# Performance work log

Hardware: AMD Instinct MI355X
Metric: run time of the kernel (lower is better)

Reference implementation:

```python
import jax, jax.numpy as jnp
import numpy as np

B, D, C, F = 1024, 8192, 345, 512
PROTO_W = 0.99  # args.proto_m


def setup_inputs() -> dict:
    key = jax.random.key(0)
    k = jax.random.split(key, 6)
    img_q = jax.random.normal(k[0], (B, D), jnp.float32)
    img_q1 = jax.random.normal(k[1], (B, D), jnp.float32)
    # partial label mask: random candidate set, guarantee >=1 candidate per row
    partial_Y = (jax.random.uniform(k[2], (B, C)) < 0.3).astype(jnp.float32)
    partial_Y = partial_Y.at[jnp.arange(B), jnp.arange(B) % C].set(1.0)
    W_enc = jax.random.normal(k[3], (D, F), jnp.float32) / np.sqrt(D).astype(np.float32)
    W_fc = jax.random.normal(k[4], (F, C), jnp.float32) / np.sqrt(F).astype(np.float32)
    b_fc = jnp.zeros((C,), jnp.float32)
    proto = jax.random.normal(k[5], (C, F), jnp.float32)
    proto = proto / jnp.linalg.norm(proto, axis=1, keepdims=True)
    return {"img_q": img_q, "img_q1": img_q1, "partial_Y": partial_Y,
            "W_enc": W_enc, "W_fc": W_fc, "b_fc": b_fc, "proto": proto}


def reference(img_q, img_q1, partial_Y, W_enc, W_fc, b_fc, proto):
    # encoder: feats [B,F], logits [B,C] (abstracted backbone + shared fc)
    feats_q = img_q @ W_enc
    logits_q = feats_q @ W_fc + b_fc
    feats_q1 = img_q1 @ W_enc
    logits_q1 = feats_q1 @ W_fc + b_fc

    # partial-label restricted pseudo labels
    scores = jax.nn.softmax(logits_q, axis=1) * partial_Y
    scores = scores / scores.sum(axis=1, keepdims=True)
    labels = jnp.argmax(scores, axis=1)  # [B] int

    # Sequential per-sample EMA p[l] = w*p[l] + (1-w)*f, vectorized in closed form.
    # For a sample with c_after same-label samples occurring later, its final
    # contribution is (1-w)*w^c_after * f; the old prototype is scaled by w^count.
    onehot = jax.nn.one_hot(labels, C, dtype=feats_q.dtype)   # [B,C]
    cum = jnp.cumsum(onehot, axis=0)                          # inclusive counts
    occ = cum[jnp.arange(B), labels] - 1.0                    # occurrences before i
    total = cum[-1]                                           # [C] per-class counts
    c_after = total[labels] - occ - 1.0                       # [B]
    coef = (1.0 - PROTO_W) * PROTO_W ** c_after               # [B]
    contrib = jax.ops.segment_sum(coef[:, None] * feats_q, labels, num_segments=C)
    new_proto = (PROTO_W ** total)[:, None] * proto + contrib
    new_proto = new_proto / jnp.linalg.norm(new_proto, axis=1, keepdims=True)

    prot_scores = new_proto @ W_fc + b_fc
    return logits_q, logits_q1, new_proto, prot_scores, labels, feats_q, feats_q1
```

## Files before the change

### kernel.cpp

```cpp
#include <hip/hip_runtime.h>
#include <float.h>
#include <math.h>

#define B_SZ 1024
#define D_SZ 8192
#define C_SZ 345
#define F_SZ 512
#define PROTO_W 0.99f


#define WS_XH 0
#define WS_XL 33554432u
#define WS_WH 67108864u
#define WS_WL 75497472u
#define WS_P  83886080u
#define WS2_WFH 100663296u
#define WS2_WFL 101056512u
#define WS2_LAB 101449728u
#define WS2_NEED 101457920u
#define WS2_FH 0u
#define WS2_FL 2097152u

#define WS_NEED 92274688u
#define WS_FH  0u
#define WS_FL  2097152u
// ... 41 lines not shown
    do {                                                                 \
        bf16x8 a0h = *(const bf16x8*)&sAh[IA0];                          \
        bf16x8 a1h = *(const bf16x8*)&sAh[IA1];                          \
        bf16x8 b0h = *(const bf16x8*)&sBh[IB0];                          \
        bf16x8 b1h = *(const bf16x8*)&sBh[IB1];                          \
        bf16x8 a0l = *(const bf16x8*)&sAl[IA0];                          \
        bf16x8 a1l = *(const bf16x8*)&sAl[IA1];                          \
        bf16x8 b0l = *(const bf16x8*)&sBl[IB0];                          \
        bf16x8 b1l = *(const bf16x8*)&sBl[IB1];                          \
        acc[0][0] = MFMA_BF16(a0h, b0h, acc[0][0], 0, 0, 0);             \
        acc[0][1] = MFMA_BF16(a0h, b1h, acc[0][1], 0, 0, 0);             \
        acc[1][0] = MFMA_BF16(a1h, b0h, acc[1][0], 0, 0, 0);             \
        acc[1][1] = MFMA_BF16(a1h, b1h, acc[1][1], 0, 0, 0);             \
        acc[0][0] = MFMA_BF16(a0h, b0l, acc[0][0], 0, 0, 0);             \
        acc[0][1] = MFMA_BF16(a0h, b1l, acc[0][1], 0, 0, 0);             \
        acc[1][0] = MFMA_BF16(a1h, b0l, acc[1][0], 0, 0, 0);             \
        acc[1][1] = MFMA_BF16(a1h, b1l, acc[1][1], 0, 0, 0);             \
        acc[0][0] = MFMA_BF16(a0l, b0h, acc[0][0], 0, 0, 0);             \
        acc[0][1] = MFMA_BF16(a0l, b1h, acc[0][1], 0, 0, 0);             \
        acc[1][0] = MFMA_BF16(a1l, b0h, acc[1][0], 0, 0, 0);             \
        acc[1][1] = MFMA_BF16(a1l, b1h, acc[1][1], 0, 0, 0);             \
    } while (0)

__global__ __launch_bounds__(256) void convert_all(
    const float* __restrict__ img_q, const float* __restrict__ img_q1,
    const float* __restrict__ W_enc, const float* __restrict__ W_fc,
    short* __restrict__ Xh, short* __restrict__ Xl,
    short* __restrict__ Wh, short* __restrict__ Wl,
    short* __restrict__ Wth, short* __restrict__ Wtl)
{
    __shared__ float tile[64][65];
    const int bid = blockIdx.x;
    const int t = threadIdx.x;

    if (bid < 1024) {
        const int HALF = (B_SZ * D_SZ) / 4;
        const int total = 2 * HALF;
        for (int i4 = bid * 256 + t; i4 < total; i4 += 1024 * 256) {
            float4 v = (i4 < HALF) ? ((const float4*)img_q)[i4]
                                   : ((const float4*)img_q1)[i4 - HALF];
            short4v h, l;
            short hh, ll;
            split_bf16(v.x, hh, ll); h.x = hh; l.x = ll;
            split_bf16(v.y, hh, ll); h.y = hh; l.y = ll;
            split_bf16(v.z, hh, ll); h.z = hh; l.z = ll;
            split_bf16(v.w, hh, ll); h.w = hh; l.w = ll;
            ((short4v*)Xh)[i4] = h;
            ((short4v*)Xl)[i4] = l;
        }
    } else if (bid < 2048) {
        const int id = bid - 1024;
        const int k0 = (id >> 3) * 64;
        const int n0 = (id & 7) * 64;
        {
            const int kr = t >> 2;
            const int cb = (t & 3) * 16;
// ... 30 lines not shown
            const int kr = idx >> 6;
            const int cc = idx & 63;
            tile[kr][cc] = (c0 + cc < C_SZ) ? W_fc[(size_t)(k0 + kr) * C_SZ + c0 + cc] : 0.0f;
        }
        __syncthreads();
        const int crow = t >> 2;
#pragma unroll
        for (int cc2 = 0; cc2 < 2; ++cc2) {
            const int ch = (t & 3) * 2 + cc2;
            short8v h, l;
#pragma unroll
            for (int e = 0; e < 8; ++e) {
                short hh, ll;
                split_bf16(tile[ch * 8 + e][crow], hh, ll);
                h[e] = hh; l[e] = ll;
            }
            size_t off = (size_t)(c0 + crow) * F_SZ + k0 + ch * 8;
            *(short8v*)&Wth[off] = h;
            *(short8v*)&Wtl[off] = l;
        }
    }
}

__global__ __launch_bounds__(512, 1) void gemm_ws128_v3(
    const short* __restrict__ Xh, const short* __restrict__ Xl,
    const short* __restrict__ Wh, const short* __restrict__ Wl,
    float* __restrict__ P, int ksteps)
{
    __shared__ __align__(16) short sAh[2][8192];
    __shared__ __align__(16) short sAl[2][8192];
    __shared__ __align__(16) short sBh[2][8192];
    __shared__ __align__(16) short sBl[2][8192];

    const int t = threadIdx.x;
    const int lane = t & 63;
    const int wave = t >> 6;

    const int flat = blockIdx.x + 4 * blockIdx.y + 64 * blockIdx.z;
    const int logical = (flat & 7) * 32 + (flat >> 3);
    const int nt = logical & 3;
    const int mt = (logical >> 2) & 15;
    const int ks = logical >> 6;

    const int m0 = mt * 128;
    const int n0 = nt * 128;
    const int kbase = ks * ksteps * 64;

    const int arr = wave >> 1;
    const int half = wave & 1;
    const short* gbase =
        (arr == 0) ? Xh + (size_t)m0 * D_SZ :
        (arr == 1) ? Xl + (size_t)m0 * D_SZ :
        (arr == 2) ? Wh + (size_t)n0 * D_SZ :
                     Wl + (size_t)n0 * D_SZ;
    short* lb[2];
    lb[0] = ((arr == 0) ? sAh[0] : (arr == 1) ? sAl[0] : (arr == 2) ? sBh[0] : sBl[0]) + half * 4096;
    lb[1] = ((arr == 0) ? sAh[1] : (arr == 1) ? sAl[1] : (arr == 2) ? sBh[1] : sBl[1]) + half * 4096;
    const int lrow8 = lane >> 3;
    const int gchunkOff = ((lane & 7) ^ lrow8) * 8;
    const short* gsrc = gbase + (size_t)(half * 64 + lrow8) * D_SZ + kbase + gchunkOff;

    const int wr = wave >> 2;
    const int wc = wave & 3;
    const int mo = wr * 64;
    const int no = wc * 32;
    const int lr = lane & 15;
    const int lkg = lane >> 4;
    const int x7 = lr & 7;
    const int sl0 = lkg ^ x7;
    const int sl1 = (4 + lkg) ^ x7;
    int aoff[4], boff[2];
#pragma unroll
    for (int f = 0; f < 4; ++f) aoff[f] = (mo + 16 * f + lr) * 64;
#pragma unroll
    for (int g = 0; g < 2; ++g) boff[g] = (no + 16 * g + lr) * 64;

    f32x4 acc[4][2] = {};

#pragma unroll
    for (int j = 0; j < 8; ++j)
        gl_lds16(gsrc + (size_t)(8 * j) * D_SZ, lb[0] + j * 512);

    int buf = 0;
    for (int s = 0; s < ksteps; ++s) {
        if (s + 1 < ksteps) {
            short* dst = lb[buf ^ 1];
            const short* g = gsrc + (s + 1) * 64;
#pragma unroll
            for (int j = 0; j < 8; ++j)
                gl_lds16(g + (size_t)(8 * j) * D_SZ, dst + j * 512);
            asm volatile("s_waitcnt vmcnt(8)" ::: "memory");
        } else {
            asm volatile("s_waitcnt vmcnt(0)" ::: "memory");
        }
        fence_barrier();

        const short* pAh = sAh[buf];
        const short* pAl = sAl[buf];
        const short* pBh = sBh[buf];
        const short* pBl = sBl[buf];

        {
            bf16x8 ah[4], al[4], bh[2], bl_[2];
#pragma unroll
            for (int f = 0; f < 4; ++f) {
                ah[f] = *(const bf16x8*)&pAh[aoff[f] + sl0 * 8];
                al[f] = *(const bf16x8*)&pAl[aoff[f] + sl0 * 8];
            }
#pragma unroll
            for (int g = 0; g < 2; ++g) {
                bh[g]  = *(const bf16x8*)&pBh[boff[g] + sl0 * 8];
                bl_[g] = *(const bf16x8*)&pBl[boff[g] + sl0 * 8];
            }
            __builtin_amdgcn_s_setprio(1);
#pragma unroll
            for (int f = 0; f < 4; ++f)
#pragma unroll
                for (int g = 0; g < 2; ++g)
                    acc[f][g] = MFMA_BF16(ah[f], bh[g], acc[f][g], 0, 0, 0);
#pragma unroll
            for (int f = 0; f < 4; ++f)
#pragma unroll
                for (int g = 0; g < 2; ++g)
                    acc[f][g] = MFMA_BF16(ah[f], bl_[g], acc[f][g], 0, 0, 0);
#pragma unroll
            for (int f = 0; f < 4; ++f)
#pragma unroll
                for (int g = 0; g < 2; ++g)
                    acc[f][g] = MFMA_BF16(al[f], bh[g], acc[f][g], 0, 0, 0);
            __builtin_amdgcn_s_setprio(0);
        }
        fence_barrier();

        {
            bf16x8 ah[4], al[4], bh[2], bl_[2];
#pragma unroll
            for (int f = 0; f < 4; ++f) {
                ah[f] = *(const bf16x8*)&pAh[aoff[f] + sl1 * 8];
                al[f] = *(const bf16x8*)&pAl[aoff[f] + sl1 * 8];
            }
#pragma unroll
            for (int g = 0; g < 2; ++g) {
                bh[g]  = *(const bf16x8*)&pBh[boff[g] + sl1 * 8];
                bl_[g] = *(const bf16x8*)&pBl[boff[g] + sl1 * 8];
            }
            __builtin_amdgcn_s_setprio(1);
#pragma unroll
            for (int f = 0; f < 4; ++f)
#pragma unroll
                for (int g = 0; g < 2; ++g)
                    acc[f][g] = MFMA_BF16(ah[f], bh[g], acc[f][g], 0, 0, 0);
#pragma unroll
            for (int f = 0; f < 4; ++f)
#pragma unroll
                for (int g = 0; g < 2; ++g)
                    acc[f][g] = MFMA_BF16(ah[f], bl_[g], acc[f][g], 0, 0, 0);
#pragma unroll
            for (int f = 0; f < 4; ++f)
#pragma unroll
                for (int g = 0; g < 2; ++g)
                    acc[f][g] = MFMA_BF16(al[f], bh[g], acc[f][g], 0, 0, 0);
            __builtin_amdgcn_s_setprio(0);
        }
        fence_barrier();
        buf ^= 1;
    }

    float* Pout = P + (size_t)ks * (2048u * 512u);
#pragma unroll
    for (int f = 0; f < 4; ++f)
#pragma unroll
        for (int g = 0; g < 2; ++g) {
            const int col  = n0 + no + 16 * g + (lane & 15);
            const int row0 = m0 + mo + 16 * f + (lane >> 4) * 4;
#pragma unroll
            for (int r = 0; r < 4; ++r)
                Pout[(size_t)(row0 + r) * F_SZ + col] = acc[f][g][r];
        }
}

__global__ __launch_bounds__(256, 1) void gemm_ws128(
    const short* __restrict__ Xh, const short* __restrict__ Xl,
    const short* __restrict__ Wh, const short* __restrict__ Wl,
    float* __restrict__ P, int ksteps)
{
    __shared__ __align__(16) short sAh[2][8192];
    __shared__ __align__(16) short sAl[2][8192];
    __shared__ __align__(16) short sBh[2][8192];
    __shared__ __align__(16) short sBl[2][8192];

    const int t = threadIdx.x;
    const int lane = t & 63;
    const int wave = t >> 6;
    const int nt = blockIdx.x;
    const int mt = blockIdx.y;
    const int ks = blockIdx.z;
    const int m0 = mt * 128;
    const int n0 = nt * 128;
    const int kbase = ks * ksteps * 64;

    const short* gbase =
        (wave == 0) ? Xh + (size_t)m0 * D_SZ :
        (wave == 1) ? Xl + (size_t)m0 * D_SZ :
// ... 73 lines not shown
#pragma unroll
                for (int f = 0; f < 4; ++f)
#pragma unroll
                    for (int g = 0; g < 4; ++g)
                        acc[f][g] = MFMA_BF16(al[f], bh[g], acc[f][g], 0, 0, 0);
            }
        }
        __builtin_amdgcn_s_setprio(0);
        fence_barrier();
        buf ^= 1;
    }

    float* Pout = P + (size_t)ks * (2048u * 512u);
#pragma unroll
    for (int f = 0; f < 4; ++f)
#pragma unroll
        for (int g = 0; g < 4; ++g) {
            const int col  = n0 + no + 16 * g + (lane & 15);
            const int row0 = m0 + mo + 16 * f + (lane >> 4) * 4;
#pragma unroll
            for (int r = 0; r < 4; ++r)
                Pout[(size_t)(row0 + r) * F_SZ + col] = acc[f][g][r];
        }
}

__global__ __launch_bounds__(256) void reduce_feats4(
    const float* __restrict__ P, float* __restrict__ feats,
    short* __restrict__ Fh, short* __restrict__ Fl)
{
    const int i4 = blockIdx.x * 256 + threadIdx.x;
    float4 a = ((const float4*)P)[i4];
#pragma unroll
    for (int sl = 1; sl < 4; ++sl) {
        float4 b = ((const float4*)(P + (size_t)sl * (2048u * 512u)))[i4];
        a.x += b.x; a.y += b.y; a.z += b.z; a.w += b.w;
    }
    ((float4*)feats)[i4] = a;
    float v[4] = {a.x, a.y, a.z, a.w};
    short4v h, l;
    short hh, ll;
#pragma unroll
    for (int e = 0; e < 4; ++e) {
        split_bf16(v[e], hh, ll); h[e] = hh; l[e] = ll;
    }
    ((short4v*)Fh)[i4] = h;
    ((short4v*)Fl)[i4] = l;
}

__global__ __launch_bounds__(256, 2) void fc_logits3(
    const short* __restrict__ Ah, const short* __restrict__ Al,
    const short* __restrict__ Bh_g, const short* __restrict__ Bl_g,
    const float* __restrict__ bias, const float* __restrict__ partial_Y,
    float* __restrict__ logits, unsigned long long* __restrict__ labPack)
{
    __shared__ __align__(16) short dAh[2][4096];
    __shared__ __align__(16) short dAl[2][4096];
    __shared__ __align__(16) short dBh[2][4096];
    __shared__ __align__(16) short dBl[2][4096];

    const int t = threadIdx.x;
    const int lane = t & 63;
    const int wave = t >> 6;
    const int n0 = blockIdx.x * 64;
    const int m0 = blockIdx.y * 64;

    const int lrow8 = lane >> 3;
    const int colOff = ((lane & 7) ^ lrow8) * 8;

    const short* gsrc = (wave == 0) ? Ah : (wave == 1) ? Al
                      : (wave == 2) ? Bh_g : Bl_g;
    const int rbase = (wave < 2) ? m0 : n0;
    short* lb[2];
    lb[0] = (wave == 0) ? dAh[0] : (wave == 1) ? dAl[0] : (wave == 2) ? dBh[0] : dBl[0];
    lb[1] = (wave == 0) ? dAh[1] : (wave == 1) ? dAl[1] : (wave == 2) ? dBh[1] : dBl[1];
    const short* gbase = gsrc + (size_t)(rbase + lrow8) * F_SZ + colOff;

    const int mo = (wave >> 1) * 32;
    const int no = (wave & 1) * 32;
    const int lr = lane & 15;
    const int lkg = lane >> 4;
    const int x7 = lr & 7;
    const int sl0 = (0 + lkg) ^ x7;
    const int sl1 = (4 + lkg) ^ x7;
    const int ra0 = (mo + lr) * 64,      ra1 = (mo + 16 + lr) * 64;
    const int rb0 = (no + lr) * 64,      rb1 = (no + 16 + lr) * 64;
    const int a00 = ra0 + sl0 * 8, a01 = ra0 + sl1 * 8;
    const int a10 = ra1 + sl0 * 8, a11 = ra1 + sl1 * 8;
    const int b00 = rb0 + sl0 * 8, b01 = rb0 + sl1 * 8;
    const int b10 = rb1 + sl0 * 8, b11 = rb1 + sl1 * 8;

    f32x4 acc[2][2] = {};

#pragma unroll
    for (int j = 0; j < 8; ++j)
        gl_lds16(gbase + (size_t)(8 * j) * F_SZ, lb[0] + j * 512);

    int buf = 0;
    for (int s = 0; s < 8; ++s) {
        if (s + 1 < 8) {
            short* dst = lb[buf ^ 1];
            const short* g = gbase + (s + 1) * 64;
#pragma unroll
            for (int j = 0; j < 8; ++j)
                gl_lds16(g + (size_t)(8 * j) * F_SZ, dst + j * 512);
            asm volatile("s_waitcnt vmcnt(8)" ::: "memory");
        } else {
            asm volatile("s_waitcnt vmcnt(0)" ::: "memory");
        }
        fence_barrier();
        __builtin_amdgcn_s_setprio(1);
        {
            const short* sAh = dAh[buf];
            const short* sAl = dAl[buf];
            const short* sBh = dBh[buf];
            const short* sBl = dBl[buf];
            MFMA_BLOCK(a00, a10, b00, b10);
            MFMA_BLOCK(a01, a11, b01, b11);
        }
        __builtin_amdgcn_s_setprio(0);
        fence_barrier();
        buf ^= 1;
    }

    const bool doArg = (m0 < B_SZ);
#pragma unroll
    for (int f = 0; f < 2; ++f) {
#pragma unroll
        for (int r = 0; r < 4; ++r) {
            const int row = m0 + mo + f * 16 + (lane >> 4) * 4 + r;
            unsigned long long best = 0;
#pragma unroll
            for (int g = 0; g < 2; ++g) {
                const int col = n0 + no + g * 16 + (lane & 15);
                if (col < C_SZ) {
                    const float v = acc[f][g][r] + bias[col];
                    logits[(size_t)row * C_SZ + col] = v;
                    if (doArg && partial_Y[(size_t)row * C_SZ + col] != 0.0f) {
                        unsigned long long p = ((unsigned long long)f2key(v) << 32)
                                             | (unsigned long long)(0xFFFFFFFFu - (unsigned)col);
                        if (p > best) best = p;
                    }
                }
            }
            if (doArg) {
#pragma unroll
                for (int m = 1; m < 16; m <<= 1) {
                    unsigned long long o = __shfl_xor(best, m);
                    if (o > best) best = o;
                }
                if ((lane & 15) == 0 && best != 0)
                    atomicMax(&labPack[row], best);
            }
        }
    }
}

__global__ __launch_bounds__(512) void proto_scores_fused(
    const unsigned long long* __restrict__ labPack,
    const float* __restrict__ feats_q,
    const float* __restrict__ proto,
    const short* __restrict__ Wth, const short* __restrict__ Wtl,
    const float* __restrict__ b_fc,
    float* __restrict__ new_proto, float* __restrict__ scores,
    float* __restrict__ labels_f)
{
    __shared__ int rowlist[B_SZ];
    __shared__ int mcount_s;
    __shared__ float nprow[F_SZ];
    __shared__ float red[8];
    __shared__ float rinv_s;
    const int c = blockIdx.x;
    const int t = threadIdx.x;
    const int lane = t & 63;
    const int w = t >> 6;

    if (c == 0) {
#pragma unroll
        for (int j = 0; j < 2; ++j) {
            const int i = t + j * 512;
            int li = (int)(0xFFFFFFFFu - (unsigned)(labPack[i] & 0xFFFFFFFFull));
            labels_f[i] = (float)li;
        }
    }

    if (w == 0) {
        int k = 0;
#pragma unroll
        for (int ch = 0; ch < 16; ++ch) {
            unsigned long long pk = labPack[ch * 64 + lane];
            int li = (int)(0xFFFFFFFFu - (unsigned)(pk & 0xFFFFFFFFull));
            unsigned long long mask = __ballot(li == c);
            if (lane == 0) {
                while (mask) {
                    int p = __builtin_ctzll(mask);
                    mask &= mask - 1;
                    rowlist[k++] = ch * 64 + p;
                }
            }
            k = __shfl(k, 0);
        }
        if (lane == 0) mcount_s = k;
    }
    __syncthreads();
    const int m = mcount_s;

    float val = proto[(size_t)c * F_SZ + t];
    for (int k = 0; k < m; ++k)
        val = PROTO_W * val + (1.0f - PROTO_W) * feats_q[(size_t)rowlist[k] * F_SZ + t];

    float sq = val * val;
#pragma unroll
    for (int off = 32; off; off >>= 1) sq += __shfl_down(sq, off);
    if ((t & 63) == 0) red[t >> 6] = sq;
    __syncthreads();
    if (t == 0) {
        float s = 0.0f;
#pragma unroll
        for (int ww = 0; ww < 8; ++ww) s += red[ww];
        rinv_s = 1.0f / sqrtf(s);
    }
    __syncthreads();
    const float v = val * rinv_s;
    new_proto[(size_t)c * F_SZ + t] = v;
    nprow[t] = v;
    __syncthreads();

    float np8[8];
#pragma unroll
    for (int j = 0; j < 8; ++j) np8[j] = nprow[lane * 8 + j];
    for (int col = w; col < C_SZ; col += 8) {
        const short8v h = *(const short8v*)&Wth[(size_t)col * F_SZ + lane * 8];
        const short8v l = *(const short8v*)&Wtl[(size_t)col * F_SZ + lane * 8];
        float p = 0.0f;
#pragma unroll
        for (int j = 0; j < 8; ++j)
            p += np8[j] * (bf16_f32(h[j]) + bf16_f32(l[j]));
#pragma unroll
        for (int off = 32; off; off >>= 1) p += __shfl_down(p, off);
        if (lane == 0) scores[(size_t)c * C_SZ + col] = p + b_fc[col];
    }
}

__global__ __launch_bounds__(256) void reduce_feats_split(
    const float* __restrict__ P, float* __restrict__ feats,
    short* __restrict__ Fh, short* __restrict__ Fl,
    const float* __restrict__ W_fc,
    short* __restrict__ Wth, short* __restrict__ Wtl)
{
    const int bid = blockIdx.x;
    const int t = threadIdx.x;
    if (bid < 1024) {
        const int n4 = (2048 * 512) / 4;
        const float* P1 = P + 2048 * 512;
        for (int i4 = bid * 256 + t; i4 < n4; i4 += 1024 * 256) {
            float4 a = ((const float4*)P)[i4];
            float4 b = ((const float4*)P1)[i4];
            float v[4] = {a.x + b.x, a.y + b.y, a.z + b.z, a.w + b.w};
            short4v h, l;
            short hh, ll;
#pragma unroll
            for (int e = 0; e < 4; ++e) {
                feats[i4 * 4 + e] = v[e];
                split_bf16(v[e], hh, ll); h[e] = hh; l[e] = ll;
// ... 183 lines not shown
    const float* proto     = (const float*)d_in[6];

    float* out       = (float*)d_out;
    float* logits    = out;
    float* new_proto = out + 706560;
    float* scores    = out + 883200;
    float* labels_f  = out + 1002225;
    float* feats     = out + 1003249;

    char* ws = (char*)d_ws;
    short* Xh = (short*)(ws + WS_XH);
    short* Xl = (short*)(ws + WS_XL);
    short* Wh = (short*)(ws + WS_WH);
    short* Wl = (short*)(ws + WS_WL);
    float* P  = (float*)(ws + WS_P);

    if (ws_size >= (size_t)WS2_NEED) {
        short* Wth = (short*)(ws + WS2_WFH);
        short* Wtl = (short*)(ws + WS2_WFL);
        unsigned long long* labPack = (unsigned long long*)(ws + WS2_LAB);
        short* Fh = (short*)(ws + WS2_FH);
        short* Fl = (short*)(ws + WS2_FL);

        hipMemsetAsync(labPack, 0, B_SZ * sizeof(unsigned long long), stream);
        hipLaunchKernelGGL(convert_all, dim3(2096), dim3(256), 0, stream,
                           img_q, img_q1, W_enc, W_fc, Xh, Xl, Wh, Wl, Wth, Wtl);
        hipLaunchKernelGGL(gemm_ws128_v3, dim3(4, 16, 4), dim3(512), 0, stream,
                           Xh, Xl, Wh, Wl, P, 32);
        hipLaunchKernelGGL(reduce_feats4, dim3(1024), dim3(256), 0, stream,
                           P, feats, Fh, Fl);
        hipLaunchKernelGGL(fc_logits3, dim3(6, 32), dim3(256), 0, stream,
                           Fh, Fl, Wth, Wtl, b_fc, partial_Y, logits, labPack);
        hipLaunchKernelGGL(proto_scores_fused, dim3(345), dim3(512), 0, stream,
                           labPack, feats, proto, Wth, Wtl, b_fc,
                           new_proto, scores, labels_f);
    } else {
        short* Fh  = (short*)(ws + WS_FH);
        short* Fl  = (short*)(ws + WS_FL);
        short* Wth = (short*)(ws + WS_WFH);
        short* Wtl = (short*)(ws + WS_WFL);
        short* NPh = (short*)(ws + WS_NPH);
        short* NPl = (short*)(ws + WS_NPL);

        hipLaunchKernelGGL(convert_all, dim3(2048), dim3(256), 0, stream,
                           img_q, img_q1, W_enc, W_fc, Xh, Xl, Wh, Wl,
                           (short*)nullptr, (short*)nullptr);
        hipLaunchKernelGGL(gemm_ws128, dim3(4, 16, 2), dim3(256), 0, stream,
                           Xh, Xl, Wh, Wl, P, 64);
        hipLaunchKernelGGL(reduce_feats_split, dim3(1072), dim3(256), 0, stream,
                           P, feats, Fh, Fl, W_fc, Wth, Wtl);
        hipLaunchKernelGGL(gemm_fc, dim3(6, 32), dim3(256), 0, stream,
                           Fh, Fl, Wth, Wtl, b_fc, logits, 2048);
        hipLaunchKernelGGL(argmax_labels, dim3(1024), dim3(64), 0, stream,
                           logits, partial_Y, labels_f);
        hipLaunchKernelGGL(proto_update, dim3(345), dim3(512), 0, stream,
                           labels_f, feats, proto, new_proto, NPh, NPl);
        hipLaunchKernelGGL(gemm_fc, dim3(6, 6), dim3(256), 0, stream,
                           NPh, NPl, Wth, Wtl, b_fc, scores, C_SZ);
    }
}
```

Baseline: 248.2 us.

## Fuse pipeline into single cooperative persistent kernel with grid syncs

Replaces the memset plus five separate launches (convert, split-K GEMM, reduce, fc logits/argmax, proto update/scores) with one cooperative kernel of 256 blocks that separates stages with grid.sync. This removes per-launch overhead and inter-kernel gaps. The cost is that each stage is limited to 256 blocks of 512 threads with one block per CU. The conversion and reduce phases lose the wider grids they had before, and the grid-wide barriers add latency of their own.

```diff
diff --git a/kernel.cpp b/kernel.cpp
--- a/kernel.cpp
+++ b/kernel.cpp
@@ -1,6 +1,9 @@
 #include <hip/hip_runtime.h>
+#include <hip/hip_cooperative_groups.h>
 #include <float.h>
 #include <math.h>
+
+namespace cg = cooperative_groups;
 
 #define B_SZ 1024
 #define D_SZ 8192
@@ -88,16 +91,503 @@
         acc[1][1] = MFMA_BF16(a1l, b1h, acc[1][1], 0, 0, 0);             \
     } while (0)
 
+__device__ __forceinline__ void proto_one(
+    int c, int t, int lane, int w,
+    const unsigned long long* labPack, const float* feats_q,
+    const float* proto_in, const short* Wth, const short* Wtl,
+    const float* b_fc, float* new_proto, float* scores, float* labels_f,
+    int* rowlist, float* nprow, float* red, int* mcount, float* rinv)
+{
+    if (c == 0) {
+#pragma unroll
+        for (int j = 0; j < 2; ++j) {
+            const int i = t + j * 512;
+            int li = (int)(0xFFFFFFFFu - (unsigned)(labPack[i] & 0xFFFFFFFFull));
+            labels_f[i] = (float)li;
+        }
+    }
+
+    if (w == 0) {
+        int k = 0;
+#pragma unroll
+        for (int ch = 0; ch < 16; ++ch) {
+            unsigned long long pk = labPack[ch * 64 + lane];
+            int li = (int)(0xFFFFFFFFu - (unsigned)(pk & 0xFFFFFFFFull));
+            unsigned long long mask = __ballot(li == c);
+            if (lane == 0) {
+                while (mask) {
+                    int p = __builtin_ctzll(mask);
+                    mask &= mask - 1;
+                    rowlist[k++] = ch * 64 + p;
+                }
+            }
+            k = __shfl(k, 0);
+        }
+        if (lane == 0) *mcount = k;
+    }
+    __syncthreads();
+    const int m = *mcount;
+
+    float val = proto_in[(size_t)c * F_SZ + t];
+    for (int k = 0; k < m; ++k)
+        val = PROTO_W * val + (1.0f - PROTO_W) * feats_q[(size_t)rowlist[k] * F_SZ + t];
+
+    float sq = val * val;
+#pragma unroll
+    for (int off = 32; off; off >>= 1) sq += __shfl_down(sq, off);
+    if ((t & 63) == 0) red[t >> 6] = sq;
+    __syncthreads();
+    if (t == 0) {
+        float s = 0.0f;
+#pragma unroll
+        for (int ww = 0; ww < 8; ++ww) s += red[ww];
+        *rinv = 1.0f / sqrtf(s);
+    }
+    __syncthreads();
+    const float v = val * (*rinv);
+    new_proto[(size_t)c * F_SZ + t] = v;
+    nprow[t] = v;
+    __syncthreads();
+
+    float np8[8];
+#pragma unroll
+    for (int j = 0; j < 8; ++j) np8[j] = nprow[lane * 8 + j];
+    for (int col = w; col < C_SZ; col += 8) {
+        const short8v h = *(const short8v*)&Wth[(size_t)col * F_SZ + lane * 8];
+        const short8v l = *(const short8v*)&Wtl[(size_t)col * F_SZ + lane * 8];
+        float p = 0.0f;
+#pragma unroll
+        for (int j = 0; j < 8; ++j)
+            p += np8[j] * (bf16_f32(h[j]) + bf16_f32(l[j]));
+#pragma unroll
+        for (int off = 32; off; off >>= 1) p += __shfl_down(p, off);
+        if (lane == 0) scores[(size_t)c * C_SZ + col] = p + b_fc[col];
+    }
+}
+
+__global__ __launch_bounds__(512, 1) void mega(
+    const float* img_q, const float* img_q1, const float* partial_Y,
+    const float* W_enc, const float* W_fc, const float* b_fc,
+    const float* proto_in,
+    short* Xh, short* Xl, short* Wh, short* Wl, float* P,
+    short* Wth, short* Wtl, unsigned long long* labPack,
+    short* Fh, short* Fl,
+    float* logits, float* new_proto, float* scores, float* labels_f,
+    float* feats)
+{
+    cg::grid_group grid = cg::this_grid();
+    __shared__ __align__(16) char LDSU[131072];
+
+    const int bid = blockIdx.x;
+    const int t = threadIdx.x;
+    const int lane = t & 63;
+    const int wave = t >> 6;
+
+    if (bid < 2) labPack[bid * 512 + t] = 0ull;
+
+    {
+        const int HALF = (B_SZ * D_SZ) / 4;
+        const int total = 2 * HALF;
+        for (int i4 = bid * 512 + t; i4 < total; i4 += 256 * 512) {
+            float4 v = (i4 < HALF) ? ((const float4*)img_q)[i4]
+                                   : ((const float4*)img_q1)[i4 - HALF];
+            short4v h, l;
+            short hh, ll;
+            split_bf16(v.x, hh, ll); h.x = hh; l.x = ll;
+            split_bf16(v.y, hh, ll); h.y = hh; l.y = ll;
+            split_bf16(v.z, hh, ll); h.z = hh; l.z = ll;
+            split_bf16(v.w, hh, ll); h.w = hh; l.w = ll;
+            ((short4v*)Xh)[i4] = h;
+            ((short4v*)Xl)[i4] = l;
+        }
+    }
+
+    {
+        float (*tile)[65] = (float(*)[65])LDSU;
+        const int kr = t >> 3;
+        const int cb = (t & 7) * 8;
+        const int n  = t >> 3;
+        const int ch = t & 7;
+#pragma unroll
+        for (int j = 0; j < 4; ++j) {
+            const int id = bid * 4 + j;
+            const int k0 = (id >> 3) * 64;
+            const int n0 = (id & 7) * 64;
+            __syncthreads();
+            float4 v0 = *(const float4*)&W_enc[(size_t)(k0 + kr) * F_SZ + n0 + cb];
+            float4 v1 = *(const float4*)&W_enc[(size_t)(k0 + kr) * F_SZ + n0 + cb + 4];
+            tile[kr][cb + 0] = v0.x; tile[kr][cb + 1] = v0.y;
+            tile[kr][cb + 2] = v0.z; tile[kr][cb + 3] = v0.w;
+            tile[kr][cb + 4] = v1.x; tile[kr][cb + 5] = v1.y;
+            tile[kr][cb + 6] = v1.z; tile[kr][cb + 7] = v1.w;
+            __syncthreads();
+            short8v h, l;
+#pragma unroll
+            for (int e = 0; e < 8; ++e) {
+                short hh, ll;
+                split_bf16(tile[ch * 8 + e][n], hh, ll);
+                h[e] = hh; l[e] = ll;
+            }
+            size_t off = (size_t)(n0 + n) * D_SZ + k0 + ch * 8;
+            *(short8v*)&Wh[off] = h;
+            *(short8v*)&Wl[off] = l;
+        }
+    }
+
+    if (bid < 48) {
+        float (*tile)[65] = (float(*)[65])LDSU;
+        const int k0 = (bid & 7) * 64;
+        const int c0 = (bid >> 3) * 64;
+        __syncthreads();
+        for (int idx = t; idx < 64 * 64; idx += 512) {
+            const int kr2 = idx >> 6;
+            const int cc = idx & 63;
+            tile[kr2][cc] = (c0 + cc < C_SZ) ? W_fc[(size_t)(k0 + kr2) * C_SZ + c0 + cc] : 0.0f;
+        }
+        __syncthreads();
+        const int crow = t >> 3;
+        const int ch2 = t & 7;
+        short8v h, l;
+#pragma unroll
+        for (int e = 0; e < 8; ++e) {
+            short hh, ll;
+            split_bf16(tile[ch2 * 8 + e][crow], hh, ll);
+            h[e] = hh; l[e] = ll;
+        }
+        size_t off = (size_t)(c0 + crow) * F_SZ + k0 + ch2 * 8;
+        *(short8v*)&Wth[off] = h;
+        *(short8v*)&Wtl[off] = l;
+    }
+
+    asm volatile("s_waitcnt vmcnt(0)" ::: "memory");
+    __threadfence();
+    grid.sync();
+
+    {
+        short (*sAh)[8192] = (short(*)[8192])(LDSU + 0);
+        short (*sAl)[8192] = (short(*)[8192])(LDSU + 32768);
+        short (*sBh)[8192] = (short(*)[8192])(LDSU + 65536);
+        short (*sBl)[8192] = (short(*)[8192])(LDSU + 98304);
+        const int ksteps = 32;
+
+        const int logical = (bid & 7) * 32 + (bid >> 3);
+        const int nt = logical & 3;
+        const int mt = (logical >> 2) & 15;
+        const int ks = logical >> 6;
+
+        const int m0 = mt * 128;
+        const int n0 = nt * 128;
+        const int kbase = ks * ksteps * 64;
+
+        const int arr = wave >> 1;
+        const int half = wave & 1;
+        const short* gbase =
+            (arr == 0) ? Xh + (size_t)m0 * D_SZ :
+            (arr == 1) ? Xl + (size_t)m0 * D_SZ :
+            (arr == 2) ? Wh + (size_t)n0 * D_SZ :
+                         Wl + (size_t)n0 * D_SZ;
+        short* lb[2];
+        lb[0] = ((arr == 0) ? sAh[0] : (arr == 1) ? sAl[0] : (arr == 2) ? sBh[0] : sBl[0]) + half * 4096;
+        lb[1] = ((arr == 0) ? sAh[1] : (arr == 1) ? sAl[1] : (arr == 2) ? sBh[1] : sBl[1]) + half * 4096;
+        const int lrow8 = lane >> 3;
+        const int gchunkOff = ((lane & 7) ^ lrow8) * 8;
+        const short* gsrc = gbase + (size_t)(half * 64 + lrow8) * D_SZ + kbase + gchunkOff;
+
+        const int wr = wave >> 2;
+        const int wc = wave & 3;
+        const int mo = wr * 64;
+        const int no = wc * 32;
+        const int lr = lane & 15;
+        const int lkg = lane >> 4;
+        const int x7 = lr & 7;
+        const int sl0 = lkg ^ x7;
+        const int sl1 = (4 + lkg) ^ x7;
+        int aoff[4], boff[2];
+#pragma unroll
+        for (int f = 0; f < 4; ++f) aoff[f] = (mo + 16 * f + lr) * 64;
+#pragma unroll
+        for (int g = 0; g < 2; ++g) boff[g] = (no + 16 * g + lr) * 64;
+
+        f32x4 acc[4][2] = {};
+
+#pragma unroll
+        for (int j = 0; j < 8; ++j)
+            gl_lds16(gsrc + (size_t)(8 * j) * D_SZ, lb[0] + j * 512);
+
+        int buf = 0;
+        for (int s = 0; s < ksteps; ++s) {
+            if (s + 1 < ksteps) {
+                short* dst = lb[buf ^ 1];
+                const short* g = gsrc + (s + 1) * 64;
+#pragma unroll
+                for (int j = 0; j < 8; ++j)
+                    gl_lds16(g + (size_t)(8 * j) * D_SZ, dst + j * 512);
+                asm volatile("s_waitcnt vmcnt(8)" ::: "memory");
+            } else {
+                asm volatile("s_waitcnt vmcnt(0)" ::: "memory");
+            }
+            fence_barrier();
+
+            const short* pAh = sAh[buf];
+            const short* pAl = sAl[buf];
+            const short* pBh = sBh[buf];
+            const short* pBl = sBl[buf];
+
+            {
+                bf16x8 ah[4], al[4], bh[2], bl_[2];
+#pragma unroll
+                for (int f = 0; f < 4; ++f) {
+                    ah[f] = *(const bf16x8*)&pAh[aoff[f] + sl0 * 8];
+                    al[f] = *(const bf16x8*)&pAl[aoff[f] + sl0 * 8];
+                }
+#pragma unroll
+                for (int g = 0; g < 2; ++g) {
+                    bh[g]  = *(const bf16x8*)&pBh[boff[g] + sl0 * 8];
+                    bl_[g] = *(const bf16x8*)&pBl[boff[g] + sl0 * 8];
+                }
+                __builtin_amdgcn_s_setprio(1);
+#pragma unroll
+                for (int f = 0; f < 4; ++f)
+#pragma unroll
+                    for (int g = 0; g < 2; ++g)
+                        acc[f][g] = MFMA_BF16(ah[f], bh[g], acc[f][g], 0, 0, 0);
+#pragma unroll
+                for (int f = 0; f < 4; ++f)
+#pragma unroll
+                    for (int g = 0; g < 2; ++g)
+                        acc[f][g] = MFMA_BF16(ah[f], bl_[g], acc[f][g], 0, 0, 0);
+#pragma unroll
+                for (int f = 0; f < 4; ++f)
+#pragma unroll
+                    for (int g = 0; g < 2; ++g)
+                        acc[f][g] = MFMA_BF16(al[f], bh[g], acc[f][g], 0, 0, 0);
+                __builtin_amdgcn_s_setprio(0);
+            }
+            fence_barrier();
+
+            {
+                bf16x8 ah[4], al[4], bh[2], bl_[2];
+#pragma unroll
+                for (int f = 0; f < 4; ++f) {
+                    ah[f] = *(const bf16x8*)&pAh[aoff[f] + sl1 * 8];
+                    al[f] = *(const bf16x8*)&pAl[aoff[f] + sl1 * 8];
+                }
+#pragma unroll
+                for (int g = 0; g < 2; ++g) {
+                    bh[g]  = *(const bf16x8*)&pBh[boff[g] + sl1 * 8];
+                    bl_[g] = *(const bf16x8*)&pBl[boff[g] + sl1 * 8];
+                }
+                __builtin_amdgcn_s_setprio(1);
+#pragma unroll
+                for (int f = 0; f < 4; ++f)
+#pragma unroll
+                    for (int g = 0; g < 2; ++g)
+                        acc[f][g] = MFMA_BF16(ah[f], bh[g], acc[f][g], 0, 0, 0);
+#pragma unroll
+                for (int f = 0; f < 4; ++f)
+#pragma unroll
+                    for (int g = 0; g < 2; ++g)
+                        acc[f][g] = MFMA_BF16(ah[f], bl_[g], acc[f][g], 0, 0, 0);
+#pragma unroll
+                for (int f = 0; f < 4; ++f)
+#pragma unroll
+                    for (int g = 0; g < 2; ++g)
+                        acc[f][g] = MFMA_BF16(al[f], bh[g], acc[f][g], 0, 0, 0);
+                __builtin_amdgcn_s_setprio(0);
+            }
+            fence_barrier();
+            buf ^= 1;
+        }
+
+        float* Pout = P + (size_t)ks * (2048u * 512u);
+#pragma unroll
+        for (int f = 0; f < 4; ++f)
+#pragma unroll
+            for (int g = 0; g < 2; ++g) {
+                const int col  = n0 + no + 16 * g + (lane & 15);
+                const int row0 = m0 + mo + 16 * f + (lane >> 4) * 4;
+#pragma unroll
+                for (int r = 0; r < 4; ++r)
+                    Pout[(size_t)(row0 + r) * F_SZ + col] = acc[f][g][r];
+            }
+    }
+
+    asm volatile("s_waitcnt vmcnt(0)" ::: "memory");
+    __threadfence();
+    grid.sync();
+
+    {
+        const int n4 = (2048 * 512) / 4;
+        for (int i4 = bid * 512 + t; i4 < n4; i4 += 256 * 512) {
+            float4 a = ((const float4*)P)[i4];
+#pragma unroll
+            for (int sl = 1; sl < 4; ++sl) {
+                float4 b = ((const float4*)(P + (size_t)sl * (2048u * 512u)))[i4];
+                a.x += b.x; a.y += b.y; a.z += b.z; a.w += b.w;
+            }
+            ((float4*)feats)[i4] = a;
+            float v[4] = {a.x, a.y, a.z, a.w};
+            short4v h, l;
+            short hh, ll;
+#pragma unroll
+            for (int e = 0; e < 4; ++e) {
+                split_bf16(v[e], hh, ll); h[e] = hh; l[e] = ll;
+            }
+            ((short4v*)Fh)[i4] = h;
+            ((short4v*)Fl)[i4] = l;
+        }
+    }
+
+    asm volatile("s_waitcnt vmcnt(0)" ::: "memory");
+    __threadfence();
+    grid.sync();
+
+    if (bid < 192) {
+        short* dAh = (short*)(LDSU + 0);
+        short* dAl = (short*)(LDSU + 16384);
+        short* dBh = (short*)(LDSU + 32768);
+        short* dBl = (short*)(LDSU + 49152);
+
+        const int n0 = (bid % 6) * 64;
+        const int m0 = (bid / 6) * 64;
+
+        const int lrow8 = lane >> 3;
+        const int colOff = ((lane & 7) ^ lrow8) * 8;
+        const int arr = wave >> 1;
+        const int halfw = wave & 1;
+        const short* gsrc = (arr == 0) ? Fh : (arr == 1) ? Fl
+                          : (arr == 2) ? Wth : Wtl;
+        const int rbase = (arr < 2) ? m0 : n0;
+        short* abase = (arr == 0) ? dAh : (arr == 1) ? dAl : (arr == 2) ? dBh : dBl;
+        short* lb[2];
+        lb[0] = abase + halfw * 2048;
+        lb[1] = abase + 4096 + halfw * 2048;
+        const short* gb = gsrc + (size_t)(rbase + halfw * 32 + lrow8) * F_SZ + colOff;
+
+        const int mo = (wave >> 1) * 16;
+        const int no_ = (wave & 1) * 32;
+        const int lr = lane & 15;
+        const int lkg = lane >> 4;
+        const int x7 = lr & 7;
+        const int sl0 = lkg ^ x7;
+        const int sl1 = (4 + lkg) ^ x7;
+        const int ra  = (mo + lr) * 64;
+        const int rb0 = (no_ + lr) * 64;
+        const int rb1 = (no_ + 16 + lr) * 64;
+
+        f32x4 acc0 = {}, acc1 = {};
+
+#pragma unroll
+        for (int j = 0; j < 4; ++j)
+            gl_lds16(gb + (size_t)(8 * j) * F_SZ, lb[0] + j * 512);
+
+        int buf = 0;
+        for (int s = 0; s < 8; ++s) {
+            if (s + 1 < 8) {
+                short* dst = lb[buf ^ 1];
+                const short* g = gb + (s + 1) * 64;
+#pragma unroll
+                for (int j = 0; j < 4; ++j)
+                    gl_lds16(g + (size_t)(8 * j) * F_SZ, dst + j * 512);
+                asm volatile("s_waitcnt vmcnt(4)" ::: "memory");
+            } else {
+                asm volatile("s_waitcnt vmcnt(0)" ::: "memory");
+            }
+            fence_barrier();
+            const short* pAh = dAh + buf * 4096;
+            const short* pAl = dAl + buf * 4096;
+            const short* pBh = dBh + buf * 4096;
+            const short* pBl = dBl + buf * 4096;
+            __builtin_amdgcn_s_setprio(1);
+#pragma unroll
+            for (int ksub = 0; ksub < 2; ++ksub) {
+                const int sl = ksub ? sl1 : sl0;
+                bf16x8 ah  = *(const bf16x8*)&pAh[ra + sl * 8];
+                bf16x8 al  = *(const bf16x8*)&pAl[ra + sl * 8];
+                bf16x8 b0h = *(const bf16x8*)&pBh[rb0 + sl * 8];
+                bf16x8 b1h = *(const bf16x8*)&pBh[rb1 + sl * 8];
+                bf16x8 b0l = *(const bf16x8*)&pBl[rb0 + sl * 8];
+                bf16x8 b1l = *(const bf16x8*)&pBl[rb1 + sl * 8];
+                acc0 = MFMA_BF16(ah, b0h, acc0, 0, 0, 0);
+                acc1 = MFMA_BF16(ah, b1h, acc1, 0, 0, 0);
+                acc0 = MFMA_BF16(ah, b0l, acc0, 0, 0, 0);
+                acc1 = MFMA_BF16(ah, b1l, acc1, 0, 0, 0);
+                acc0 = MFMA_BF16(al, b0h, acc0, 0, 0, 0);
+                acc1 = MFMA_BF16(al, b1h, acc1, 0, 0, 0);
+            }
+            __builtin_amdgcn_s_setprio(0);
+            fence_barrier();
+            buf ^= 1;
+        }
+
+        const bool doArg = (m0 < B_SZ);
+#pragma unroll
+        for (int r = 0; r < 4; ++r) {
+            const int row = m0 + mo + lkg * 4 + r;
+            unsigned long long best = 0;
+#pragma unroll
+            for (int g = 0; g < 2; ++g) {
+                const int col = n0 + no_ + g * 16 + lr;
+                if (col < C_SZ) {
+                    const float v = (g ? acc1[r] : acc0[r]) + b_fc[col];
+                    logits[(size_t)row * C_SZ + col] = v;
+                    if (doArg && partial_Y[(size_t)row * C_SZ + col] != 0.0f) {
+                        unsigned long long pk = ((unsigned long long)f2key(v) << 32)
+                                              | (unsigned long long)(0xFFFFFFFFu - (unsigned)col);
+                        if (pk > best) best = pk;
+                    }
+                }
+            }
+            if (doArg) {
+#pragma unroll
+                for (int mm = 1; mm < 16; mm <<= 1) {
+                    unsigned long long o = __shfl_xor(best, mm);
+                    if (o > best) best = o;
+                }
+                if (lr == 0 && best != 0)
+                    atomicMax(&labPack[row], best);
+            }
+        }
+    }
+
+    asm volatile("s_waitcnt vmcnt(0)" ::: "memory");
+    __threadfence();
+    grid.sync();
+
+    {
+        int*   rowlist = (int*)LDSU;
+        float* nprow   = (float*)(LDSU + 4096);
+        float* red     = (float*)(LDSU + 6144);
+        int*   mcount  = (int*)(LDSU + 6176);
+        float* rinv    = (float*)(LDSU + 6180);
+
+        proto_one(bid, t, lane, wave, labPack, feats, proto_in, Wth, Wtl,
+                  b_fc, new_proto, scores, labels_f,
+                  rowlist, nprow, red, mcount, rinv);
+        const int c2 = bid + 256;
+        if (c2 < C_SZ) {
+            __syncthreads();
+            proto_one(c2, t, lane, wave, labPack, feats, proto_in, Wth, Wtl,
+                      b_fc, new_proto, scores, labels_f,
+                      rowlist, nprow, red, mcount, rinv);
+        }
+    }
+}
+
 __global__ __launch_bounds__(256) void convert_all(
     const float* __restrict__ img_q, const float* __restrict__ img_q1,
     const float* __restrict__ W_enc, const float* __restrict__ W_fc,
     short* __restrict__ Xh, short* __restrict__ Xl,
     short* __restrict__ Wh, short* __restrict__ Wl,
-    short* __restrict__ Wth, short* __restrict__ Wtl)
+    short* __restrict__ Wth, short* __restrict__ Wtl,
+    unsigned long long* __restrict__ labPack)
 {
     __shared__ float tile[64][65];
     const int bid = blockIdx.x;
     const int t = threadIdx.x;
+
+    if (labPack && bid < 4)
+        labPack[bid * 256 + t] = 0ull;
 
     if (bid < 1024) {
         const int HALF = (B_SZ * D_SZ) / 4;
@@ -174,163 +664,6 @@
     }
 }
 
-__global__ __launch_bounds__(512, 1) void gemm_ws128_v3(
-    const short* __restrict__ Xh, const short* __restrict__ Xl,
-    const short* __restrict__ Wh, const short* __restrict__ Wl,
-    float* __restrict__ P, int ksteps)
-{
-    __shared__ __align__(16) short sAh[2][8192];
-    __shared__ __align__(16) short sAl[2][8192];
-    __shared__ __align__(16) short sBh[2][8192];
-    __shared__ __align__(16) short sBl[2][8192];
-
-    const int t = threadIdx.x;
-    const int lane = t & 63;
-    const int wave = t >> 6;
-
-    const int flat = blockIdx.x + 4 * blockIdx.y + 64 * blockIdx.z;
-    const int logical = (flat & 7) * 32 + (flat >> 3);
-    const int nt = logical & 3;
-    const int mt = (logical >> 2) & 15;
-    const int ks = logical >> 6;
-
-    const int m0 = mt * 128;
-    const int n0 = nt * 128;
-    const int kbase = ks * ksteps * 64;
-
-    const int arr = wave >> 1;
-    const int half = wave & 1;
-    const short* gbase =
-        (arr == 0) ? Xh + (size_t)m0 * D_SZ :
-        (arr == 1) ? Xl + (size_t)m0 * D_SZ :
-        (arr == 2) ? Wh + (size_t)n0 * D_SZ :
-                     Wl + (size_t)n0 * D_SZ;
-    short* lb[2];
-    lb[0] = ((arr == 0) ? sAh[0] : (arr == 1) ? sAl[0] : (arr == 2) ? sBh[0] : sBl[0]) + half * 4096;
-    lb[1] = ((arr == 0) ? sAh[1] : (arr == 1) ? sAl[1] : (arr == 2) ? sBh[1] : sBl[1]) + half * 4096;
-    const int lrow8 = lane >> 3;
-    const int gchunkOff = ((lane & 7) ^ lrow8) * 8;
-    const short* gsrc = gbase + (size_t)(half * 64 + lrow8) * D_SZ + kbase + gchunkOff;
-
-    const int wr = wave >> 2;
-    const int wc = wave & 3;
-    const int mo = wr * 64;
-    const int no = wc * 32;
-    const int lr = lane & 15;
-    const int lkg = lane >> 4;
-    const int x7 = lr & 7;
-    const int sl0 = lkg ^ x7;
-    const int sl1 = (4 + lkg) ^ x7;
-    int aoff[4], boff[2];
-#pragma unroll
-    for (int f = 0; f < 4; ++f) aoff[f] = (mo + 16 * f + lr) * 64;
-#pragma unroll
-    for (int g = 0; g < 2; ++g) boff[g] = (no + 16 * g + lr) * 64;
-
-    f32x4 acc[4][2] = {};
-
-#pragma unroll
-    for (int j = 0; j < 8; ++j)
-        gl_lds16(gsrc + (size_t)(8 * j) * D_SZ, lb[0] + j * 512);
-
-    int buf = 0;
-    for (int s = 0; s < ksteps; ++s) {
-        if (s + 1 < ksteps) {
-            short* dst = lb[buf ^ 1];
-            const short* g = gsrc + (s + 1) * 64;
-#pragma unroll
-            for (int j = 0; j < 8; ++j)
-                gl_lds16(g + (size_t)(8 * j) * D_SZ, dst + j * 512);
-            asm volatile("s_waitcnt vmcnt(8)" ::: "memory");
-        } else {
-            asm volatile("s_waitcnt vmcnt(0)" ::: "memory");
-        }
-        fence_barrier();
-
-        const short* pAh = sAh[buf];
-        const short* pAl = sAl[buf];
-        const short* pBh = sBh[buf];
-        const short* pBl = sBl[buf];
-
-        {
-            bf16x8 ah[4], al[4], bh[2], bl_[2];
-#pragma unroll
-            for (int f = 0; f < 4; ++f) {
-                ah[f] = *(const bf16x8*)&pAh[aoff[f] + sl0 * 8];
-                al[f] = *(const bf16x8*)&pAl[aoff[f] + sl0 * 8];
-            }
-#pragma unroll
-            for (int g = 0; g < 2; ++g) {
-                bh[g]  = *(const bf16x8*)&pBh[boff[g] + sl0 * 8];
-                bl_[g] = *(const bf16x8*)&pBl[boff[g] + sl0 * 8];
-            }
-            __builtin_amdgcn_s_setprio(1);
-#pragma unroll
-            for (int f = 0; f < 4; ++f)
-#pragma unroll
-                for (int g = 0; g < 2; ++g)
-                    acc[f][g] = MFMA_BF16(ah[f], bh[g], acc[f][g], 0, 0, 0);
-#pragma unroll
-            for (int f = 0; f < 4; ++f)
-#pragma unroll
-                for (int g = 0; g < 2; ++g)
-                    acc[f][g] = MFMA_BF16(ah[f], bl_[g], acc[f][g], 0, 0, 0);
-#pragma unroll
-            for (int f = 0; f < 4; ++f)
-#pragma unroll
-                for (int g = 0; g < 2; ++g)
-                    acc[f][g] = MFMA_BF16(al[f], bh[g], acc[f][g], 0, 0, 0);
-            __builtin_amdgcn_s_setprio(0);
-        }
-        fence_barrier();
-
-        {
-            bf16x8 ah[4], al[4], bh[2], bl_[2];
-#pragma unroll
-            for (int f = 0; f < 4; ++f) {
-                ah[f] = *(const bf16x8*)&pAh[aoff[f] + sl1 * 8];
-                al[f] = *(const bf16x8*)&pAl[aoff[f] + sl1 * 8];
-            }
-#pragma unroll
-            for (int g = 0; g < 2; ++g) {
-                bh[g]  = *(const bf16x8*)&pBh[boff[g] + sl1 * 8];
-                bl_[g] = *(const bf16x8*)&pBl[boff[g] + sl1 * 8];
-            }
-            __builtin_amdgcn_s_setprio(1);
-#pragma unroll
-            for (int f = 0; f < 4; ++f)
-#pragma unroll
-                for (int g = 0; g < 2; ++g)
-                    acc[f][g] = MFMA_BF16(ah[f], bh[g], acc[f][g], 0, 0, 0);
-#pragma unroll
-            for (int f = 0; f < 4; ++f)
-#pragma unroll
-                for (int g = 0; g < 2; ++g)
-                    acc[f][g] = MFMA_BF16(ah[f], bl_[g], acc[f][g], 0, 0, 0);
-#pragma unroll
-            for (int f = 0; f < 4; ++f)
-#pragma unroll
-                for (int g = 0; g < 2; ++g)
-                    acc[f][g] = MFMA_BF16(al[f], bh[g], acc[f][g], 0, 0, 0);
-            __builtin_amdgcn_s_setprio(0);
-        }
-        fence_barrier();
-        buf ^= 1;
-    }
-
-    float* Pout = P + (size_t)ks * (2048u * 512u);
-#pragma unroll
-    for (int f = 0; f < 4; ++f)
-#pragma unroll
-        for (int g = 0; g < 2; ++g) {
-            const int col  = n0 + no + 16 * g + (lane & 15);
-            const int row0 = m0 + mo + 16 * f + (lane >> 4) * 4;
-#pragma unroll
-            for (int r = 0; r < 4; ++r)
-                Pout[(size_t)(row0 + r) * F_SZ + col] = acc[f][g][r];
-        }
-}
-
 __global__ __launch_bounds__(256, 1) void gemm_ws128(
     const short* __restrict__ Xh, const short* __restrict__ Xl,
     const short* __restrict__ Wh, const short* __restrict__ Wl,
@@ -450,223 +783,6 @@
             for (int r = 0; r < 4; ++r)
                 Pout[(size_t)(row0 + r) * F_SZ + col] = acc[f][g][r];
         }
-}
-
-__global__ __launch_bounds__(256) void reduce_feats4(
-    const float* __restrict__ P, float* __restrict__ feats,
-    short* __restrict__ Fh, short* __restrict__ Fl)
-{
-    const int i4 = blockIdx.x * 256 + threadIdx.x;
-    float4 a = ((const float4*)P)[i4];
-#pragma unroll
-    for (int sl = 1; sl < 4; ++sl) {
-        float4 b = ((const float4*)(P + (size_t)sl * (2048u * 512u)))[i4];
-        a.x += b.x; a.y += b.y; a.z += b.z; a.w += b.w;
-    }
-    ((float4*)feats)[i4] = a;
-    float v[4] = {a.x, a.y, a.z, a.w};
-    short4v h, l;
-    short hh, ll;
-#pragma unroll
-    for (int e = 0; e < 4; ++e) {
-        split_bf16(v[e], hh, ll); h[e] = hh; l[e] = ll;
-    }
-    ((short4v*)Fh)[i4] = h;
-    ((short4v*)Fl)[i4] = l;
-}
-
-__global__ __launch_bounds__(256, 2) void fc_logits3(
-    const short* __restrict__ Ah, const short* __restrict__ Al,
-    const short* __restrict__ Bh_g, const short* __restrict__ Bl_g,
-    const float* __restrict__ bias, const float* __restrict__ partial_Y,
-    float* __restrict__ logits, unsigned long long* __restrict__ labPack)
-{
-    __shared__ __align__(16) short dAh[2][4096];
-    __shared__ __align__(16) short dAl[2][4096];
-    __shared__ __align__(16) short dBh[2][4096];
-    __shared__ __align__(16) short dBl[2][4096];
-
-    const int t = threadIdx.x;
-    const int lane = t & 63;
-    const int wave = t >> 6;
-    const int n0 = blockIdx.x * 64;
-    const int m0 = blockIdx.y * 64;
-
-    const int lrow8 = lane >> 3;
-    const int colOff = ((lane & 7) ^ lrow8) * 8;
-
-    const short* gsrc = (wave == 0) ? Ah : (wave == 1) ? Al
-                      : (wave == 2) ? Bh_g : Bl_g;
-    const int rbase = (wave < 2) ? m0 : n0;
-    short* lb[2];
-    lb[0] = (wave == 0) ? dAh[0] : (wave == 1) ? dAl[0] : (wave == 2) ? dBh[0] : dBl[0];
-    lb[1] = (wave == 0) ? dAh[1] : (wave == 1) ? dAl[1] : (wave == 2) ? dBh[1] : dBl[1];
-    const short* gbase = gsrc + (size_t)(rbase + lrow8) * F_SZ + colOff;
-
-    const int mo = (wave >> 1) * 32;
-    const int no = (wave & 1) * 32;
-    const int lr = lane & 15;
-    const int lkg = lane >> 4;
-    const int x7 = lr & 7;
-    const int sl0 = (0 + lkg) ^ x7;
-    const int sl1 = (4 + lkg) ^ x7;
-    const int ra0 = (mo + lr) * 64,      ra1 = (mo + 16 + lr) * 64;
-    const int rb0 = (no + lr) * 64,      rb1 = (no + 16 + lr) * 64;
-    const int a00 = ra0 + sl0 * 8, a01 = ra0 + sl1 * 8;
-    const int a10 = ra1 + sl0 * 8, a11 = ra1 + sl1 * 8;
-    const int b00 = rb0 + sl0 * 8, b01 = rb0 + sl1 * 8;
-    const int b10 = rb1 + sl0 * 8, b11 = rb1 + sl1 * 8;
-
-    f32x4 acc[2][2] = {};
-
-#pragma unroll
-    for (int j = 0; j < 8; ++j)
-        gl_lds16(gbase + (size_t)(8 * j) * F_SZ, lb[0] + j * 512);
-
-    int buf = 0;
-    for (int s = 0; s < 8; ++s) {
-        if (s + 1 < 8) {
-            short* dst = lb[buf ^ 1];
-            const short* g = gbase + (s + 1) * 64;
-#pragma unroll
-            for (int j = 0; j < 8; ++j)
-                gl_lds16(g + (size_t)(8 * j) * F_SZ, dst + j * 512);
-            asm volatile("s_waitcnt vmcnt(8)" ::: "memory");
-        } else {
-            asm volatile("s_waitcnt vmcnt(0)" ::: "memory");
-        }
-        fence_barrier();
-        __builtin_amdgcn_s_setprio(1);
-        {
-            const short* sAh = dAh[buf];
-            const short* sAl = dAl[buf];
-            const short* sBh = dBh[buf];
-            const short* sBl = dBl[buf];
-            MFMA_BLOCK(a00, a10, b00, b10);
-            MFMA_BLOCK(a01, a11, b01, b11);
-        }
-        __builtin_amdgcn_s_setprio(0);
-        fence_barrier();
-        buf ^= 1;
-    }
-
-    const bool doArg = (m0 < B_SZ);
-#pragma unroll
-    for (int f = 0; f < 2; ++f) {
-#pragma unroll
-        for (int r = 0; r < 4; ++r) {
-            const int row = m0 + mo + f * 16 + (lane >> 4) * 4 + r;
-            unsigned long long best = 0;
-#pragma unroll
-            for (int g = 0; g < 2; ++g) {
-                const int col = n0 + no + g * 16 + (lane & 15);
-                if (col < C_SZ) {
-                    const float v = acc[f][g][r] + bias[col];
-                    logits[(size_t)row * C_SZ + col] = v;
-                    if (doArg && partial_Y[(size_t)row * C_SZ + col] != 0.0f) {
-                        unsigned long long p = ((unsigned long long)f2key(v) << 32)
-                                             | (unsigned long long)(0xFFFFFFFFu - (unsigned)col);
-                        if (p > best) best = p;
-                    }
-                }
-            }
-            if (doArg) {
-#pragma unroll
-                for (int m = 1; m < 16; m <<= 1) {
-                    unsigned long long o = __shfl_xor(best, m);
-                    if (o > best) best = o;
-                }
-                if ((lane & 15) == 0 && best != 0)
-                    atomicMax(&labPack[row], best);
-            }
-        }
-    }
-}
-
-__global__ __launch_bounds__(512) void proto_scores_fused(
-    const unsigned long long* __restrict__ labPack,
-    const float* __restrict__ feats_q,
-    const float* __restrict__ proto,
-    const short* __restrict__ Wth, const short* __restrict__ Wtl,
-    const float* __restrict__ b_fc,
-    float* __restrict__ new_proto, float* __restrict__ scores,
-    float* __restrict__ labels_f)
-{
-    __shared__ int rowlist[B_SZ];
-    __shared__ int mcount_s;
-    __shared__ float nprow[F_SZ];
-    __shared__ float red[8];
-    __shared__ float rinv_s;
-    const int c = blockIdx.x;
-    const int t = threadIdx.x;
-    const int lane = t & 63;
-    const int w = t >> 6;
-
-    if (c == 0) {
-#pragma unroll
-        for (int j = 0; j < 2; ++j) {
-            const int i = t + j * 512;
-            int li = (int)(0xFFFFFFFFu - (unsigned)(labPack[i] & 0xFFFFFFFFull));
-            labels_f[i] = (float)li;
-        }
-    }
-
-    if (w == 0) {
-        int k = 0;
-#pragma unroll
-        for (int ch = 0; ch < 16; ++ch) {
-            unsigned long long pk = labPack[ch * 64 + lane];
-            int li = (int)(0xFFFFFFFFu - (unsigned)(pk & 0xFFFFFFFFull));
-            unsigned long long mask = __ballot(li == c);
-            if (lane == 0) {
-                while (mask) {
-                    int p = __builtin_ctzll(mask);
-                    mask &= mask - 1;
-                    rowlist[k++] = ch * 64 + p;
-                }
-            }
-            k = __shfl(k, 0);
-        }
-        if (lane == 0) mcount_s = k;
-    }
-    __syncthreads();
-    const int m = mcount_s;
-
-    float val = proto[(size_t)c * F_SZ + t];
-    for (int k = 0; k < m; ++k)
-        val = PROTO_W * val + (1.0f - PROTO_W) * feats_q[(size_t)rowlist[k] * F_SZ + t];
-
-    float sq = val * val;
-#pragma unroll
-    for (int off = 32; off; off >>= 1) sq += __shfl_down(sq, off);
-    if ((t & 63) == 0) red[t >> 6] = sq;
-    __syncthreads();
-    if (t == 0) {
-        float s = 0.0f;
-#pragma unroll
-        for (int ww = 0; ww < 8; ++ww) s += red[ww];
-        rinv_s = 1.0f / sqrtf(s);
-    }
-    __syncthreads();
-    const float v = val * rinv_s;
-    new_proto[(size_t)c * F_SZ + t] = v;
-    nprow[t] = v;
-    __syncthreads();
-
-    float np8[8];
-#pragma unroll
-    for (int j = 0; j < 8; ++j) np8[j] = nprow[lane * 8 + j];
-    for (int col = w; col < C_SZ; col += 8) {
-        const short8v h = *(const short8v*)&Wth[(size_t)col * F_SZ + lane * 8];
-        const short8v l = *(const short8v*)&Wtl[(size_t)col * F_SZ + lane * 8];
-        float p = 0.0f;
-#pragma unroll
-        for (int j = 0; j < 8; ++j)
-            p += np8[j] * (bf16_f32(h[j]) + bf16_f32(l[j]));
-#pragma unroll
-        for (int off = 32; off; off >>= 1) p += __shfl_down(p, off);
-        if (lane == 0) scores[(size_t)c * C_SZ + col] = p + b_fc[col];
-    }
 }
 
 __global__ __launch_bounds__(256) void reduce_feats_split(
@@ -896,18 +1012,17 @@
         short* Fh = (short*)(ws + WS2_FH);
         short* Fl = (short*)(ws + WS2_FL);
 
-        hipMemsetAsync(labPack, 0, B_SZ * sizeof(unsigned long long), stream);
-        hipLaunchKernelGGL(convert_all, dim3(2096), dim3(256), 0, stream,
-                           img_q, img_q1, W_enc, W_fc, Xh, Xl, Wh, Wl, Wth, Wtl);
-        hipLaunchKernelGGL(gemm_ws128_v3, dim3(4, 16, 4), dim3(512), 0, stream,
-                           Xh, Xl, Wh, Wl, P, 32);
-        hipLaunchKernelGGL(reduce_feats4, dim3(1024), dim3(256), 0, stream,
-                           P, feats, Fh, Fl);
-        hipLaunchKernelGGL(fc_logits3, dim3(6, 32), dim3(256), 0, stream,
-                           Fh, Fl, Wth, Wtl, b_fc, partial_Y, logits, labPack);
-        hipLaunchKernelGGL(proto_scores_fused, dim3(345), dim3(512), 0, stream,
-                           labPack, feats, proto, Wth, Wtl, b_fc,
-                           new_proto, scores, labels_f);
+        void* args[] = {
+            (void*)&img_q, (void*)&img_q1, (void*)&partial_Y,
+            (void*)&W_enc, (void*)&W_fc, (void*)&b_fc, (void*)&proto,
+            (void*)&Xh, (void*)&Xl, (void*)&Wh, (void*)&Wl, (void*)&P,
+            (void*)&Wth, (void*)&Wtl, (void*)&labPack,
+            (void*)&Fh, (void*)&Fl,
+            (void*)&logits, (void*)&new_proto, (void*)&scores,
+            (void*)&labels_f, (void*)&feats
+        };
+        hipLaunchCooperativeKernel((const void*)mega, dim3(256), dim3(512),
+                                   args, 0, stream);
     } else {
         short* Fh  = (short*)(ws + WS_FH);
         short* Fl  = (short*)(ws + WS_FL);
@@ -918,7 +1033,8 @@
 
         hipLaunchKernelGGL(convert_all, dim3(2048), dim3(256), 0, stream,
                            img_q, img_q1, W_enc, W_fc, Xh, Xl, Wh, Wl,
-                           (short*)nullptr, (short*)nullptr);
+                           (short*)nullptr, (short*)nullptr,
+                           (unsigned long long*)nullptr);
         hipLaunchKernelGGL(gemm_ws128, dim3(4, 16, 2), dim3(256), 0, stream,
                            Xh, Xl, Wh, Wl, P, 64);
         hipLaunchKernelGGL(reduce_feats_split, dim3(1072), dim3(256), 0, stream,
```

After: 614.4 us. 2.48x slower.
